# Kernel tuning notes

Hardware: AMD Instinct MI355X
Metric: run time of the kernel (lower is better)

## Reference

```python
import jax, jax.numpy as jnp
import numpy as np

N, D, R, O = 4096, 128, 256, 64


def setup_inputs() -> dict:
    key = jax.random.key(0)
    k1, k2, k3, k4 = jax.random.split(key, 4)
    X = jax.random.normal(k1, (N, D), dtype=jnp.float32)
    # Gaussian membership params per rule: centers and (positive) widths, shape [R, D]
    centers = 0.5 * jax.random.normal(k2, (R, D), dtype=jnp.float32)
    sigmas = 1.5 + jax.random.uniform(k3, (R, D), dtype=jnp.float32)  # in [1.5, 2.5]
    # Takagi-Sugeno per-rule linear coeffs [R, D+1, O] (last row = bias)
    coeffs = 0.02 * jax.random.normal(k4, (R, D + 1, O), dtype=jnp.float32)
    return {"X": X, "centers": centers, "sigmas": sigmas, "coeffs": coeffs}


def reference(X, centers, sigmas, coeffs):
    # Layer 1: Gaussian memberships for all rules at once: [N, R, D]
    diff = X[:, None, :] - centers[None, :, :]
    memb = jnp.exp(-(diff * diff) / (2.0 * sigmas * sigmas)[None, :, :])
    # Layer 2: rule strengths via product over input dims ('prod' strategy): [N, R]
    strengths = jnp.prod(memb, axis=2)
    # Layer 3: normalize across rules
    norm = strengths / (jnp.sum(strengths, axis=1, keepdims=True) + 1e-8)
    # Layer 4: per-rule linear consequents: [N, R, O]
    weighted = jnp.einsum('ni,rij->nrj', X, coeffs[:, :-1, :]) + coeffs[:, -1, :][None, :, :]
    # Layer 5: weighted combine over rules: [N, O]
    out = jnp.einsum('nr,nrj->nj', norm, weighted)
    # task='classification' -> Softmax(dim=1)
    return jax.nn.softmax(out, axis=1)
```

## Files before the change

### kernel.cpp

```cpp
#include <hip/hip_runtime.h>

#define N_SAMPLES 4096
#define D_IN      128
#define R_RULES   256
#define O_OUT     64
#define KPAD      136
#define NCHUNK    17
#define CH_I      8
#define RG        32
#define NGROUPS   8

typedef _Float16 f16;
typedef _Float16 f16x2 __attribute__((ext_vector_type(2)));
typedef _Float16 f16x8 __attribute__((ext_vector_type(8)));
typedef float    f32x4 __attribute__((ext_vector_type(4)));

__global__ __launch_bounds__(256) void anfis_strengths(
    const float* __restrict__ X, const float* __restrict__ centers,
    const float* __restrict__ sigmas, float* __restrict__ S) {
  __shared__ float Xs[32 * 129];
  __shared__ float Cs[32 * 129];
  __shared__ float Is[32 * 129];
  const int tid = threadIdx.x;
  const int n0 = blockIdx.x * 32;
  const int r0 = blockIdx.y * 32;

#pragma unroll
  for (int i = 0; i < 4; ++i) {
    int idx = tid + (i << 8);
    int m = idx >> 5, k4 = (idx & 31) << 2;
    float4 v = reinterpret_cast<const float4*>(X)[(size_t)(n0 + m) * 32 + (idx & 31)];
    float* d = &Xs[m * 129 + k4];
    d[0] = v.x; d[1] = v.y; d[2] = v.z; d[3] = v.w;
    float4 c = reinterpret_cast<const float4*>(centers)[(size_t)(r0 + m) * 32 + (idx & 31)];
    float* dc = &Cs[m * 129 + k4];
    dc[0] = c.x; dc[1] = c.y; dc[2] = c.z; dc[3] = c.w;
    float4 s = reinterpret_cast<const float4*>(sigmas)[(size_t)(r0 + m) * 32 + (idx & 31)];
    float* di = &Is[m * 129 + k4];
    di[0] = 0.5f / (s.x * s.x); di[1] = 0.5f / (s.y * s.y);
    di[2] = 0.5f / (s.z * s.z); di[3] = 0.5f / (s.w * s.w);
  }
  __syncthreads();

  const int mloc = (tid >> 4) << 1;
  const int rloc = (tid & 15) << 1;
  float e00 = 0.f, e01 = 0.f, e10 = 0.f, e11 = 0.f;
  for (int k = 0; k < 128; ++k) {
    float x0 = Xs[mloc * 129 + k];
    float x1 = Xs[(mloc + 1) * 129 + k];
    float c0 = Cs[rloc * 129 + k];
    float iv0 = Is[rloc * 129 + k];
    float c1 = Cs[(rloc + 1) * 129 + k];
    float iv1 = Is[(rloc + 1) * 129 + k];
    float d00 = x0 - c0, d01 = x0 - c1, d10 = x1 - c0, d11 = x1 - c1;
    e00 = fmaf(-(d00 * d00), iv0, e00);
    e01 = fmaf(-(d01 * d01), iv1, e01);
    e10 = fmaf(-(d10 * d10), iv0, e10);
    e11 = fmaf(-(d11 * d11), iv1, e11);
  }
  float2 v0 = make_float2(__expf(e00), __expf(e01));
  float2 v1 = make_float2(__expf(e10), __expf(e11));
  *reinterpret_cast<float2*>(&S[(size_t)(n0 + mloc) * R_RULES + r0 + rloc]) = v0;
  *reinterpret_cast<float2*>(&S[(size_t)(n0 + mloc + 1) * R_RULES + r0 + rloc]) = v1;
}

__global__ __launch_bounds__(256) void anfis_normalize(float* __restrict__ S) {
  const int n = blockIdx.x * 4 + (threadIdx.x >> 6);
  const int lane = threadIdx.x & 63;
  float4 v = reinterpret_cast<float4*>(S)[(size_t)n * 64 + lane];
  float s = (v.x + v.y) + (v.z + v.w);
#pragma unroll
  for (int off = 32; off; off >>= 1) s += __shfl_xor(s, off, 64);
  const float inv = 1.0f / (s + 1e-8f);
  v.x *= inv; v.y *= inv; v.z *= inv; v.w *= inv;
  reinterpret_cast<float4*>(S)[(size_t)n * 64 + lane] = v;
}

__global__ __launch_bounds__(256) void anfis_prep(
    const float* __restrict__ coeffs, f16* __restrict__ Cp) {
  __shared__ alignas(16) f16 T[64 * 32];
  const int i = blockIdx.x;
  const int g = blockIdx.y;
  const int tid = threadIdx.x;
  const int rg = tid & 31;
  const int jb = tid >> 5;
  if (i < 129) {
    const float* src = coeffs + ((size_t)(g * 32 + rg) * 129 + i) * 64 + jb * 8;
    float4 a = reinterpret_cast<const float4*>(src)[0];
    float4 b = reinterpret_cast<const float4*>(src)[1];
    T[(jb * 8 + 0) * 32 + rg] = (f16)a.x;
    T[(jb * 8 + 1) * 32 + rg] = (f16)a.y;
    T[(jb * 8 + 2) * 32 + rg] = (f16)a.z;
    T[(jb * 8 + 3) * 32 + rg] = (f16)a.w;
    T[(jb * 8 + 4) * 32 + rg] = (f16)b.x;
    T[(jb * 8 + 5) * 32 + rg] = (f16)b.y;
    T[(jb * 8 + 6) * 32 + rg] = (f16)b.z;
    T[(jb * 8 + 7) * 32 + rg] = (f16)b.w;
  } else {
#pragma unroll
    for (int q = 0; q < 8; ++q) T[(jb * 8 + q) * 32 + rg] = (f16)0.0f;
  }
  __syncthreads();
  f16x8* dst = reinterpret_cast<f16x8*>(
      Cp + (((size_t)g * NCHUNK + (i >> 3)) * CH_I + (i & 7)) * 2048);
  dst[tid] = reinterpret_cast<const f16x8*>(T)[tid];
}

__global__ __launch_bounds__(256) void anfis_main16(
    const float* __restrict__ X, const float* __restrict__ P,
    const f16* __restrict__ Cp, float* __restrict__ part) {
  __shared__ alignas(16) f16 Xs[KPAD * 64];
  __shared__ alignas(16) f16 Bs[CH_I * 64 * 32];
  const int tid = threadIdx.x;
  const int g = blockIdx.x & 7;
  const int m0 = (blockIdx.x >> 3) * 64;
  const int w = tid >> 6, lane = tid & 63;
  const int mg = w >> 1, ng = w & 1;
  const int lm = lane & 15, quad = lane >> 4;

#pragma unroll
  for (int it = 0; it < 8; ++it) {
    int fi = tid + (it << 8);
    int m = fi >> 5, k4 = (fi & 31) << 2;
    float4 v = reinterpret_cast<const float4*>(X)[(size_t)(m0 + m) * 32 + (fi & 31)];
    Xs[(k4 + 0) * 64 + m] = (f16)v.x;
    Xs[(k4 + 1) * 64 + m] = (f16)v.y;
    Xs[(k4 + 2) * 64 + m] = (f16)v.z;
    Xs[(k4 + 3) * 64 + m] = (f16)v.w;
  }
  if (tid < 64) {
    Xs[128 * 64 + tid] = (f16)1.0f;
#pragma unroll
    for (int ip = 129; ip < KPAD; ++ip) Xs[ip * 64 + tid] = (f16)0.0f;
  }

  union F8 { f16x8 v; f16x2 h[4]; };
  F8 pf[2];
#pragma unroll
  for (int mf = 0; mf < 2; ++mf) {
    int row = m0 + mg * 32 + mf * 16 + lm;
    const float* pp = P + (size_t)row * R_RULES + g * 32 + quad * 8;
    float4 p0 = reinterpret_cast<const float4*>(pp)[0];
    float4 p1 = reinterpret_cast<const float4*>(pp)[1];
    pf[mf].h[0] = f16x2{(f16)p0.x, (f16)p0.y};
    pf[mf].h[1] = f16x2{(f16)p0.z, (f16)p0.w};
    pf[mf].h[2] = f16x2{(f16)p1.x, (f16)p1.y};
    pf[mf].h[3] = f16x2{(f16)p1.z, (f16)p1.w};
  }

  f32x4 acc[2][2] = {};
  const char* cpg = (const char*)(Cp + (size_t)g * NCHUNK * CH_I * 2048);

  for (int c = 0; c < NCHUNK; ++c) {
    __syncthreads();
    const char* gsrc = cpg + (size_t)c * 32768;
#pragma unroll
    for (int it = 0; it < 8; ++it) {
      int off = (it << 12) + (w << 10);
      __builtin_amdgcn_global_load_lds(
          (const __attribute__((address_space(1))) unsigned int*)(gsrc + off + lane * 16),
          (__attribute__((address_space(3))) unsigned int*)((char*)Bs + off),
          16, 0, 0);
    }
    __syncthreads();
#pragma unroll
    for (int ii = 0; ii < CH_I; ++ii) {
      const int i = c * CH_I + ii;
      F8 a[2];
#pragma unroll
      for (int mf = 0; mf < 2; ++mf) {
        f16 xv = Xs[i * 64 + mg * 32 + mf * 16 + lm];
        f16x2 xd = {xv, xv};
        a[mf].h[0] = pf[mf].h[0] * xd;
        a[mf].h[1] = pf[mf].h[1] * xd;
        a[mf].h[2] = pf[mf].h[2] * xd;
        a[mf].h[3] = pf[mf].h[3] * xd;
      }
      const f16* brow = &Bs[(ii * 64 + ng * 32 + lm) * 32 + quad * 8];
      f16x8 b0 = *reinterpret_cast<const f16x8*>(brow);
      f16x8 b1 = *reinterpret_cast<const f16x8*>(brow + 16 * 32);
      acc[0][0] = __builtin_amdgcn_mfma_f32_16x16x32_f16(a[0].v, b0, acc[0][0], 0, 0, 0);
      acc[0][1] = __builtin_amdgcn_mfma_f32_16x16x32_f16(a[0].v, b1, acc[0][1], 0, 0, 0);
      acc[1][0] = __builtin_amdgcn_mfma_f32_16x16x32_f16(a[1].v, b0, acc[1][0], 0, 0, 0);
      acc[1][1] = __builtin_amdgcn_mfma_f32_16x16x32_f16(a[1].v, b1, acc[1][1], 0, 0, 0);
    }
  }

#pragma unroll
  for (int mf = 0; mf < 2; ++mf)
#pragma unroll
    for (int nf = 0; nf < 2; ++nf)
#pragma unroll
      for (int q = 0; q < 4; ++q) {
        int row = m0 + mg * 32 + mf * 16 + quad * 4 + q;
        int col = ng * 32 + nf * 16 + lm;
        part[((size_t)g * N_SAMPLES + row) * O_OUT + col] = acc[mf][nf][q];
      }
}

__global__ __launch_bounds__(256) void anfis_out(
    const float* __restrict__ part, float* __restrict__ out) {
  const int n = blockIdx.x * 4 + (threadIdx.x >> 6);
  const int lane = threadIdx.x & 63;
  const size_t stride = (size_t)N_SAMPLES * O_OUT;
  const float* p0 = part + (size_t)n * O_OUT + lane;
  float v = 0.f;
#pragma unroll
  for (int gg = 0; gg < 8; ++gg) v += p0[gg * stride];
  float mx = v;
#pragma unroll
  for (int off = 32; off; off >>= 1) mx = fmaxf(mx, __shfl_xor(mx, off, 64));
  float e = __expf(v - mx);
  float s = e;
#pragma unroll
  for (int off = 32; off; off >>= 1) s += __shfl_xor(s, off, 64);
  out[(size_t)n * O_OUT + lane] = e / s;
}

extern "C" void kernel_launch(void* const* d_in, const int* in_sizes, int n_in,
                              void* d_out, int out_size, void* d_ws, size_t ws_size,
                              hipStream_t stream) {
  const float* X       = (const float*)d_in[0];
  const float* centers = (const float*)d_in[1];
  const float* sigmas  = (const float*)d_in[2];
  const float* coeffs  = (const float*)d_in[3];
  float* out = (float*)d_out;

  float* S    = (float*)d_ws;
  float* part = S + (size_t)N_SAMPLES * R_RULES;
  f16*   Cp   = (f16*)(part + (size_t)NGROUPS * N_SAMPLES * O_OUT);

  anfis_prep<<<dim3(KPAD, NGROUPS), 256, 0, stream>>>(coeffs, Cp);
  anfis_strengths<<<dim3(N_SAMPLES / 32, R_RULES / 32), 256, 0, stream>>>(
      X, centers, sigmas, S);
  anfis_normalize<<<N_SAMPLES / 4, 256, 0, stream>>>(S);
  anfis_main16<<<512, 256, 0, stream>>>(X, S, Cp, part);
  anfis_out<<<N_SAMPLES / 4, 256, 0, stream>>>(part, out);
}
```

Baseline: 122.5 us.

## Compute Gaussian rule strengths as split-fp16 MFMA GEMM via expanded quadratic

The per-rule exponent sum -(x-c)^2/(2σ^2) is expanded into x^2·b1 + x·b2 + const, and each factor is split into hi/lo fp16 parts. This turns the strengths computation into a K≈800 fp16 MFMA GEMM against a precomputed B matrix built by a new prep kernel, replacing the scalar fp32 loop. The main kernel's X tile is also changed to a row-major layout so each thread loads 8 X values with one vector read per chunk instead of scalar LDS reads. The split-precision scheme is meant to keep accuracy, but it adds an extra prep launch and workspace, and cancellation in the expanded form could lose precision.

Measured after the change: 109.4 us. 10.7% less time.

```diff
diff --git a/kernel.cpp b/kernel.cpp
--- a/kernel.cpp
+++ b/kernel.cpp
@@ -7,61 +7,121 @@
 #define KPAD      136
 #define NCHUNK    17
 #define CH_I      8
-#define RG        32
 #define NGROUPS   8
 
 typedef _Float16 f16;
 typedef _Float16 f16x2 __attribute__((ext_vector_type(2)));
+typedef _Float16 f16x4 __attribute__((ext_vector_type(4)));
 typedef _Float16 f16x8 __attribute__((ext_vector_type(8)));
 typedef float    f32x4 __attribute__((ext_vector_type(4)));
 
-__global__ __launch_bounds__(256) void anfis_strengths(
-    const float* __restrict__ X, const float* __restrict__ centers,
-    const float* __restrict__ sigmas, float* __restrict__ S) {
-  __shared__ float Xs[32 * 129];
-  __shared__ float Cs[32 * 129];
-  __shared__ float Is[32 * 129];
+__global__ __launch_bounds__(128) void anfis_prep2(
+    const float* __restrict__ centers, const float* __restrict__ sigmas,
+    f16* __restrict__ Bext) {
+  const int r = blockIdx.x;
+  const int d = threadIdx.x;
+  const float c = centers[(size_t)r * 128 + d];
+  const float s = sigmas[(size_t)r * 128 + d];
+  const float iv = 0.5f / (s * s);
+  const float b1 = -iv;
+  const float b2 = 2.0f * c * iv;
+  f16 b1h = (f16)b1; f16 b1l = (f16)(b1 - (float)b1h);
+  f16 b2h = (f16)b2; f16 b2l = (f16)(b2 - (float)b2h);
+  auto put = [&](int k, f16 v) {
+    Bext[((size_t)(k >> 3) * 256 + r) * 8 + (k & 7)] = v;
+  };
+  put(d, b1h);
+  put(128 + d, b1l);
+  put(256 + d, b1h);
+  put(384 + d, b2h);
+  put(512 + d, b2l);
+  put(640 + d, b2h);
+  float p = -c * c * iv;
+#pragma unroll
+  for (int off = 32; off; off >>= 1) p += __shfl_xor(p, off, 64);
+  __shared__ float red[2];
+  if ((threadIdx.x & 63) == 0) red[threadIdx.x >> 6] = p;
+  __syncthreads();
+  if (d < 30) put(770 + d, (f16)0.0f);
+  if (d == 0) {
+    float k2 = red[0] + red[1];
+    f16 h = (f16)k2; f16 l = (f16)(k2 - (float)h);
+    put(768, h);
+    put(769, l);
+  }
+}
+
+__global__ __launch_bounds__(512) void anfis_s16(
+    const float* __restrict__ X, const f16* __restrict__ Bext,
+    float* __restrict__ S) {
+  __shared__ alignas(16) f16 Xq[32 * 512];
   const int tid = threadIdx.x;
-  const int n0 = blockIdx.x * 32;
-  const int r0 = blockIdx.y * 32;
-
-#pragma unroll
-  for (int i = 0; i < 4; ++i) {
-    int idx = tid + (i << 8);
-    int m = idx >> 5, k4 = (idx & 31) << 2;
-    float4 v = reinterpret_cast<const float4*>(X)[(size_t)(n0 + m) * 32 + (idx & 31)];
-    float* d = &Xs[m * 129 + k4];
-    d[0] = v.x; d[1] = v.y; d[2] = v.z; d[3] = v.w;
-    float4 c = reinterpret_cast<const float4*>(centers)[(size_t)(r0 + m) * 32 + (idx & 31)];
-    float* dc = &Cs[m * 129 + k4];
-    dc[0] = c.x; dc[1] = c.y; dc[2] = c.z; dc[3] = c.w;
-    float4 s = reinterpret_cast<const float4*>(sigmas)[(size_t)(r0 + m) * 32 + (idx & 31)];
-    float* di = &Is[m * 129 + k4];
-    di[0] = 0.5f / (s.x * s.x); di[1] = 0.5f / (s.y * s.y);
-    di[2] = 0.5f / (s.z * s.z); di[3] = 0.5f / (s.w * s.w);
+  const int m0 = (blockIdx.x >> 1) * 32;
+  const int r0 = (blockIdx.x & 1) * 128;
+  const int w = tid >> 6, lane = tid & 63;
+  const int mg = w >> 2, ng = w & 3;
+  const int lm = lane & 15, quad = lane >> 4;
+
+  {
+    int m = tid >> 4, oct = tid & 15;
+    const float* src = X + (size_t)(m0 + m) * 128 + oct * 8;
+    float4 a = reinterpret_cast<const float4*>(src)[0];
+    float4 b = reinterpret_cast<const float4*>(src)[1];
+    float xs[8] = {a.x, a.y, a.z, a.w, b.x, b.y, b.z, b.w};
+    f16x8 vh, vl, v2h, v2l;
+#pragma unroll
+    for (int q = 0; q < 8; ++q) {
+      float x = xs[q];
+      f16 h = (f16)x;   f16 l = (f16)(x - (float)h);
+      float x2 = x * x;
+      f16 h2 = (f16)x2; f16 l2 = (f16)(x2 - (float)h2);
+      vh[q] = h; vl[q] = l; v2h[q] = h2; v2l[q] = l2;
+    }
+    f16x8* row = reinterpret_cast<f16x8*>(&Xq[m * 512]);
+    int sw = m & 7;
+    row[(0 * 16 + oct) ^ sw] = v2h;
+    row[(1 * 16 + oct) ^ sw] = v2l;
+    row[(2 * 16 + oct) ^ sw] = vh;
+    row[(3 * 16 + oct) ^ sw] = vl;
   }
   __syncthreads();
 
-  const int mloc = (tid >> 4) << 1;
-  const int rloc = (tid & 15) << 1;
-  float e00 = 0.f, e01 = 0.f, e10 = 0.f, e11 = 0.f;
-  for (int k = 0; k < 128; ++k) {
-    float x0 = Xs[mloc * 129 + k];
-    float x1 = Xs[(mloc + 1) * 129 + k];
-    float c0 = Cs[rloc * 129 + k];
-    float iv0 = Is[rloc * 129 + k];
-    float c1 = Cs[(rloc + 1) * 129 + k];
-    float iv1 = Is[(rloc + 1) * 129 + k];
-    float d00 = x0 - c0, d01 = x0 - c1, d10 = x1 - c0, d11 = x1 - c1;
-    e00 = fmaf(-(d00 * d00), iv0, e00);
-    e01 = fmaf(-(d01 * d01), iv1, e01);
-    e10 = fmaf(-(d10 * d10), iv0, e10);
-    e11 = fmaf(-(d11 * d11), iv1, e11);
-  }
-  float2 v0 = make_float2(__expf(e00), __expf(e01));
-  float2 v1 = make_float2(__expf(e10), __expf(e11));
-  *reinterpret_cast<float2*>(&S[(size_t)(n0 + mloc) * R_RULES + r0 + rloc]) = v0;
-  *reinterpret_cast<float2*>(&S[(size_t)(n0 + mloc + 1) * R_RULES + r0 + rloc]) = v1;
+  f32x4 acc[2] = {};
+  const int am = mg * 16 + lm;
+  const f16x8* arow = reinterpret_cast<const f16x8*>(&Xq[am * 512]);
+  const int asw = am & 7;
+  const int col0 = r0 + ng * 32 + lm;
+
+#pragma unroll
+  for (int t = 0; t < 24; ++t) {
+    const int seg = t >> 2;
+    const int plane = (seg < 2) ? 0 : (seg == 2) ? 1 : (seg < 5) ? 2 : 3;
+    const int o = t * 4 + quad;
+    f16x8 av = arow[(plane * 16 + (o & 15)) ^ asw];
+    const f16* bp = Bext + ((size_t)o * 256 + col0) * 8;
+    f16x8 b0 = *reinterpret_cast<const f16x8*>(bp);
+    f16x8 b1 = *reinterpret_cast<const f16x8*>(bp + 16 * 8);
+    acc[0] = __builtin_amdgcn_mfma_f32_16x16x32_f16(av, b0, acc[0], 0, 0, 0);
+    acc[1] = __builtin_amdgcn_mfma_f32_16x16x32_f16(av, b1, acc[1], 0, 0, 0);
+  }
+  {
+    f16x8 av = {};
+    if (quad == 0) { av[0] = (f16)1.0f; av[1] = (f16)1.0f; }
+    const int o = 96 + quad;
+    const f16* bp = Bext + ((size_t)o * 256 + col0) * 8;
+    f16x8 b0 = *reinterpret_cast<const f16x8*>(bp);
+    f16x8 b1 = *reinterpret_cast<const f16x8*>(bp + 16 * 8);
+    acc[0] = __builtin_amdgcn_mfma_f32_16x16x32_f16(av, b0, acc[0], 0, 0, 0);
+    acc[1] = __builtin_amdgcn_mfma_f32_16x16x32_f16(av, b1, acc[1], 0, 0, 0);
+  }
+#pragma unroll
+  for (int nf = 0; nf < 2; ++nf)
+#pragma unroll
+    for (int q = 0; q < 4; ++q) {
+      int row = m0 + mg * 16 + quad * 4 + q;
+      int col = r0 + ng * 32 + nf * 16 + lm;
+      S[(size_t)row * R_RULES + col] = __expf(acc[nf][q]);
+    }
 }
 
 __global__ __launch_bounds__(256) void anfis_normalize(float* __restrict__ S) {
@@ -109,7 +169,7 @@
 __global__ __launch_bounds__(256) void anfis_main16(
     const float* __restrict__ X, const float* __restrict__ P,
     const f16* __restrict__ Cp, float* __restrict__ part) {
-  __shared__ alignas(16) f16 Xs[KPAD * 64];
+  __shared__ alignas(16) f16 Xs[64 * KPAD];
   __shared__ alignas(16) f16 Bs[CH_I * 64 * 32];
   const int tid = threadIdx.x;
   const int g = blockIdx.x & 7;
@@ -123,15 +183,13 @@
     int fi = tid + (it << 8);
     int m = fi >> 5, k4 = (fi & 31) << 2;
     float4 v = reinterpret_cast<const float4*>(X)[(size_t)(m0 + m) * 32 + (fi & 31)];
-    Xs[(k4 + 0) * 64 + m] = (f16)v.x;
-    Xs[(k4 + 1) * 64 + m] = (f16)v.y;
-    Xs[(k4 + 2) * 64 + m] = (f16)v.z;
-    Xs[(k4 + 3) * 64 + m] = (f16)v.w;
+    f16x4 h = {(f16)v.x, (f16)v.y, (f16)v.z, (f16)v.w};
+    *reinterpret_cast<f16x4*>(&Xs[m * KPAD + k4]) = h;
   }
   if (tid < 64) {
-    Xs[128 * 64 + tid] = (f16)1.0f;
-#pragma unroll
-    for (int ip = 129; ip < KPAD; ++ip) Xs[ip * 64 + tid] = (f16)0.0f;
+    f16x8 bias = {};
+    bias[0] = (f16)1.0f;
+    *reinterpret_cast<f16x8*>(&Xs[tid * KPAD + 128]) = bias;
   }
 
   union F8 { f16x8 v; f16x2 h[4]; };
@@ -163,14 +221,16 @@
           16, 0, 0);
     }
     __syncthreads();
+    f16x8 xv[2];
+    xv[0] = *reinterpret_cast<const f16x8*>(&Xs[(mg * 32 + lm) * KPAD + c * 8]);
+    xv[1] = *reinterpret_cast<const f16x8*>(&Xs[(mg * 32 + 16 + lm) * KPAD + c * 8]);
 #pragma unroll
     for (int ii = 0; ii < CH_I; ++ii) {
-      const int i = c * CH_I + ii;
       F8 a[2];
 #pragma unroll
       for (int mf = 0; mf < 2; ++mf) {
-        f16 xv = Xs[i * 64 + mg * 32 + mf * 16 + lm];
-        f16x2 xd = {xv, xv};
+        f16 xvv = xv[mf][ii];
+        f16x2 xd = {xvv, xvv};
         a[mf].h[0] = pf[mf].h[0] * xd;
         a[mf].h[1] = pf[mf].h[1] * xd;
         a[mf].h[2] = pf[mf].h[2] * xd;
@@ -229,10 +289,11 @@
   float* S    = (float*)d_ws;
   float* part = S + (size_t)N_SAMPLES * R_RULES;
   f16*   Cp   = (f16*)(part + (size_t)NGROUPS * N_SAMPLES * O_OUT);
-
+  f16*   Bext = Cp + (size_t)NGROUPS * NCHUNK * CH_I * 2048;
+
+  anfis_prep2<<<R_RULES, 128, 0, stream>>>(centers, sigmas, Bext);
   anfis_prep<<<dim3(KPAD, NGROUPS), 256, 0, stream>>>(coeffs, Cp);
-  anfis_strengths<<<dim3(N_SAMPLES / 32, R_RULES / 32), 256, 0, stream>>>(
-      X, centers, sigmas, S);
+  anfis_s16<<<256, 512, 0, stream>>>(X, Bext, S);
   anfis_normalize<<<N_SAMPLES / 4, 256, 0, stream>>>(S);
   anfis_main16<<<512, 256, 0, stream>>>(X, S, Cp, part);
   anfis_out<<<N_SAMPLES / 4, 256, 0, stream>>>(part, out);
```
